# Kernel optimization log

Hardware: AMD Instinct MI355X
Metric: run time of the kernel (lower is better)

Reference implementation:

```python
import jax, jax.numpy as jnp
import numpy as np

# Config mirrors init_kwargs
D_IN, D_OUT, HEADS, SEQ, BATCH = 1024, 64, 16, 2048, 2


def setup_inputs() -> dict:
    key = jax.random.key(0)
    kx, kq, kk, kv = jax.random.split(key, 4)
    scale = 1.0 / np.sqrt(D_IN)
    x = jax.random.normal(kx, (BATCH, SEQ, D_IN), dtype=jnp.float32)
    # Stacked per-head projection weights, [H, d_in, d_out] (qkv_bias=False)
    Wq = jax.random.normal(kq, (HEADS, D_IN, D_OUT), dtype=jnp.float32) * scale
    Wk = jax.random.normal(kk, (HEADS, D_IN, D_OUT), dtype=jnp.float32) * scale
    Wv = jax.random.normal(kv, (HEADS, D_IN, D_OUT), dtype=jnp.float32) * scale
    return {"x": x, "Wq": Wq, "Wk": Wk, "Wv": Wv}


def reference(x, Wq, Wk, Wv):
    # x: [B, S, d_in]; W*: [H, d_in, d_out]
    q = jnp.einsum("bsd,hde->bhse", x, Wq)
    k = jnp.einsum("bsd,hde->bhse", x, Wk)
    v = jnp.einsum("bsd,hde->bhse", x, Wv)
    scores = jnp.einsum("bhse,bhte->bhst", q, k) / jnp.sqrt(
        jnp.asarray(D_OUT, dtype=q.dtype)
    )
    S = x.shape[1]
    causal = jnp.tril(jnp.ones((S, S), dtype=bool))  # [S, S]
    scores = jnp.where(causal[None, None], scores, -jnp.inf)
    attn = jax.nn.softmax(scores, axis=-1)  # dropout=0.0 (eval)
    ctx = jnp.einsum("bhst,bhte->bhse", attn, v)  # [B, H, S, d_out]
    # concat heads on last dim -> [B, S, H*d_out]
    B, H, S2, E = ctx.shape
    return jnp.transpose(ctx, (0, 2, 1, 3)).reshape(B, S2, H * E)
```

## Files before the change

### kernel.cpp

```cpp
#include <hip/hip_runtime.h>
#include <hip/hip_bf16.h>
#include <math.h>

#define BATCH 2
#define SEQ   2048
#define DIN   1024
#define HEADS 16
#define EDIM  64

#define NX   (BATCH*SEQ*DIN)
#define NW   (3*HEADS*DIN*EDIM)
#define NQKV (BATCH*HEADS*SEQ*EDIM)

#define QSCALE 0.18033688011112042f

typedef __attribute__((ext_vector_type(8))) short short8;
typedef __attribute__((ext_vector_type(4))) float f32x4;

static __device__ __forceinline__ ushort f2bf(float f) {
    __hip_bfloat16 h = __float2bfloat16(f);
    return *reinterpret_cast<ushort*>(&h);
}

static __device__ __forceinline__ void gload16(const void* g, void* l) {
    void* gv = const_cast<void*>(g);
    __builtin_amdgcn_global_load_lds(
        (__attribute__((address_space(1))) void*)gv,
        (__attribute__((address_space(3))) void*)l,
        16, 0, 0);
}

static __device__ __forceinline__ void barrier_fenced() {
    asm volatile("" ::: "memory");
    __builtin_amdgcn_s_barrier();
    asm volatile("" ::: "memory");
}

__global__ __launch_bounds__(256) void prep(
    const float* __restrict__ x, const float* __restrict__ Wq,
    const float* __restrict__ Wk, const float* __restrict__ Wv,
    ushort* __restrict__ xb, ushort* __restrict__ wt)
{
    const int t = threadIdx.x;
    if (blockIdx.x < 1024) {
        const int v0 = blockIdx.x * 256 + t;
#pragma unroll
        for (int i = 0; i < 4; ++i) {
            int i4 = (v0 + i * 262144) * 4;
            float4 f = *(const float4*)(x + i4);
            ushort4 o;
            o.x = f2bf(f.x); o.y = f2bf(f.y); o.z = f2bf(f.z); o.w = f2bf(f.w);
            *(ushort4*)(xb + i4) = o;
        }
    } else {
        const int bid = blockIdx.x - 1024;
        const int dt  = bid & 15;
        const int h   = (bid >> 4) & 15;
        const int mat = bid >> 8;

        const float* W = (mat == 0) ? Wq : (mat == 1) ? Wk : Wv;
        const float* src = W + ((size_t)h * DIN + dt * 64) * EDIM;
        ushort* dst = wt + ((size_t)(mat * HEADS + h) * EDIM) * DIN + dt * 64;

        __shared__ ushort T[64][68];
#pragma unroll
        for (int i = 0; i < 16; ++i) {
            int v = t + i * 256;
            int d = v >> 6, e = v & 63;
            T[d][e] = f2bf(src[(size_t)d * EDIM + e]);
        }
        __syncthreads();
#pragma unroll
        for (int i = 0; i < 4; ++i) {
            int v = t + i * 256;
            int e = v >> 4, d4 = (v & 15) << 2;
            ushort4 ov;
            ov.x = T[d4 + 0][e]; ov.y = T[d4 + 1][e];
            ov.z = T[d4 + 2][e]; ov.w = T[d4 + 3][e];
            *(ushort4*)&dst[(size_t)e * DIN + d4] = ov;
        }
    }
}

__global__ __launch_bounds__(256) void qkv_gemm(
    const ushort* __restrict__ xb, const ushort* __restrict__ wt,
    ushort* __restrict__ qkv)
{
    const int bid = blockIdx.x;
    const int xcd = bid & 7;
    const int idx = bid >> 3;
    const int mt  = (xcd >> 1) * 8 + idx / 12;
    const int nt  = (xcd & 1) * 12 + idx % 12;
    const int m0 = mt * 128, n0 = nt * 128;
    const int b  = mt >> 4;

    __shared__ ushort As[2][128][64];
    __shared__ ushort Bs[2][128][64];

    const int t    = threadIdx.x;
    const int lane = t & 63;
    const int w    = t >> 6;
    const int wr   = w >> 1, wc = w & 1;
    const int fr   = lane & 15;
    const int fk   = (lane >> 4) * 8;
    const int rg   = (lane >> 4) * 4;
    const int sw   = (fr & 7) << 3;

    const ushort* xbase = xb + (size_t)m0 * DIN;
    const ushort* wbase = wt + (size_t)n0 * DIN;

    const int lrow = lane >> 3;
    const int lcol = ((lane & 7) ^ (lane >> 3)) << 3;

#define STAGE(buf, k0)                                                          \
    {                                                                           \
        _Pragma("unroll")                                                       \
        for (int j = 0; j < 4; ++j) {                                           \
            const int c = w * 4 + j;                                            \
            gload16(&xbase[(size_t)(c * 8 + lrow) * DIN + (k0) + lcol], &As[buf][c * 8][0]); \
            gload16(&wbase[(size_t)(c * 8 + lrow) * DIN + (k0) + lcol], &Bs[buf][c * 8][0]); \
        }                                                                       \
    }

    f32x4 acc[4][4];
#pragma unroll
    for (int i = 0; i < 4; ++i)
#pragma unroll
        for (int j = 0; j < 4; ++j) acc[i][j] = (f32x4)0.f;

    STAGE(0, 0);
    STAGE(1, 64);

    short8 a[4][2], bfr[4][2];

#define LOAD_FRAGS(cur)                                                         \
    {                                                                           \
        _Pragma("unroll")                                                       \
        for (int rb = 0; rb < 4; ++rb)                                          \
            _Pragma("unroll")                                                   \
            for (int kk = 0; kk < 2; ++kk) {                                    \
                a[rb][kk]   = *(const short8*)&As[cur][wr * 64 + rb * 16 + fr][(kk * 32 + fk) ^ sw]; \
                bfr[rb][kk] = *(const short8*)&Bs[cur][wc * 64 + rb * 16 + fr][(kk * 32 + fk) ^ sw]; \
            }                                                                   \
    }

#define DO_MFMA()                                                               \
    {                                                                           \
        _Pragma("unroll")                                                       \
        for (int kk = 0; kk < 2; ++kk)                                          \
            _Pragma("unroll")                                                   \
            for (int rb = 0; rb < 4; ++rb)                                      \
                _Pragma("unroll")                                               \
                for (int cf = 0; cf < 4; ++cf)                                  \
                    acc[rb][cf] = __builtin_amdgcn_mfma_f32_16x16x32_bf16(a[rb][kk], bfr[cf][kk], acc[rb][cf], 0, 0, 0); \
    }

    for (int kt = 0; kt < 15; ++kt) {
        const int cur = kt & 1;

        asm volatile("s_waitcnt vmcnt(8)" ::: "memory");
        __builtin_amdgcn_sched_barrier(0);
        barrier_fenced();

        LOAD_FRAGS(cur);

        asm volatile("s_waitcnt lgkmcnt(0)" ::: "memory");
        __builtin_amdgcn_sched_barrier(0);
        barrier_fenced();

        if (kt <= 13) STAGE(cur, (kt + 2) * 64);

        DO_MFMA();
    }
    {
        asm volatile("s_waitcnt vmcnt(0)" ::: "memory");
        __builtin_amdgcn_sched_barrier(0);
        barrier_fenced();
        LOAD_FRAGS(1);
        DO_MFMA();
    }
#undef STAGE
#undef LOAD_FRAGS
#undef DO_MFMA

    const int hg  = nt * 2 + wc;
    const int mat = hg >> 4;
    const int h   = hg & 15;
    const int s0  = (m0 & 2047) + wr * 64;
    if (mat < 2) {
        const float sc = (mat == 0) ? QSCALE : 1.0f;
        ushort* dst = qkv + (size_t)mat * NQKV
                    + ((size_t)((b * HEADS + h) * SEQ) + s0) * EDIM;
#pragma unroll
        for (int rb = 0; rb < 4; ++rb)
#pragma unroll
            for (int cf = 0; cf < 4; ++cf)
#pragma unroll
                for (int i = 0; i < 4; ++i)
                    dst[(size_t)(rb * 16 + rg + i) * EDIM + cf * 16 + fr] = f2bf(acc[rb][cf][i] * sc);
    } else {
        ushort* vtb = qkv + (size_t)2 * NQKV + ((size_t)(b * HEADS + h) * EDIM) * SEQ;
#pragma unroll
        for (int rb = 0; rb < 4; ++rb)
#pragma unroll
            for (int cf = 0; cf < 4; ++cf) {
                ushort4 ov;
                ov.x = f2bf(acc[rb][cf][0]); ov.y = f2bf(acc[rb][cf][1]);
                ov.z = f2bf(acc[rb][cf][2]); ov.w = f2bf(acc[rb][cf][3]);
                *(ushort4*)&vtb[(size_t)(cf * 16 + fr) * SEQ + s0 + rb * 16 + rg] = ov;
            }
    }
}

__global__ __launch_bounds__(512) void flash_mfma(
    const ushort* __restrict__ q, const ushort* __restrict__ k,
    const ushort* __restrict__ vt, float* __restrict__ out)
{
    const int bid = blockIdx.x;
    const int bh  = bid & 31;
    const int b   = bh >> 4;
    const int h   = bh & 15;
    const int it  = (bid < 256) ? (15 - (bid >> 5)) : ((bid - 256) >> 5);
    const int KT  = 2 * it + 2;

    const ushort* Qb  = q  + ((size_t)((b * HEADS + h) * SEQ) + it * 128) * EDIM;
    const ushort* Kb  = k  + ((size_t)((b * HEADS + h) * SEQ)) * EDIM;
    const ushort* Vtb = vt + ((size_t)((b * HEADS + h) * EDIM)) * SEQ;

    __shared__ ushort Ks_[2][64][64];
    __shared__ ushort Vs_[2][64][64];
    __shared__ ushort Ps_[8][16][72];

    const int t    = threadIdx.x;
    const int lane = t & 63;
    const int w    = t >> 6;
    const int fr   = lane & 15;
    const int fk   = (lane >> 4) * 8;
    const int rg   = (lane >> 4) * 4;
    const int sw   = (fr & 7) << 3;

    const int srow8 = lane >> 3;
    const int sunit = (lane & 7) ^ srow8;

#define FSTAGE(buf, tile)                                                      \
    {                                                                          \
        gload16(&Kb[(size_t)((tile) * 64 + w * 8 + srow8) * EDIM + sunit * 8], \
                &Ks_[buf][w * 8][0]);                                          \
        gload16(&Vtb[(size_t)(w * 8 + srow8) * SEQ + (tile) * 64 + sunit * 8], \
                &Vs_[buf][w * 8][0]);                                          \
    }

    const int wrow0 = it * 128 + w * 16;
    const int lastT = wrow0 >> 6;
    const int qrow  = wrow0 + fr;

    short8 qf[2];
#pragma unroll
    for (int kk = 0; kk < 2; ++kk)
        qf[kk] = *(const short8*)&Qb[(size_t)(w * 16 + fr) * EDIM + kk * 32 + fk];
    asm volatile("s_waitcnt vmcnt(0)" ::: "memory");
    __builtin_amdgcn_sched_barrier(0);

    f32x4 o_[4];
#pragma unroll
    for (int cf = 0; cf < 4; ++cf) o_[cf] = (f32x4)0.f;
    float lpart = 0.f;

    FSTAGE(0, 0);

    for (int kt = 0; kt < KT; ++kt) {
        const int cur = kt & 1;

        asm volatile("s_waitcnt vmcnt(0)" ::: "memory");
        __builtin_amdgcn_sched_barrier(0);
        barrier_fenced();

        if (kt + 1 < KT) FSTAGE(cur ^ 1, kt + 1);

        if (kt <= lastT) {
            f32x4 s[4];
#pragma unroll
            for (int cf = 0; cf < 4; ++cf) s[cf] = (f32x4)0.f;
#pragma unroll
            for (int cf = 0; cf < 4; ++cf)
#pragma unroll
                for (int kk = 0; kk < 2; ++kk) {
                    short8 kf = *(const short8*)&Ks_[cur][cf * 16 + fr][(kk * 32 + fk) ^ sw];
                    s[cf] = __builtin_amdgcn_mfma_f32_16x16x32_bf16(kf, qf[kk], s[cf], 0, 0, 0);
                }

            if (kt == lastT) {
#pragma unroll
                for (int cf = 0; cf < 4; ++cf)
#pragma unroll
                    for (int i = 0; i < 4; ++i) {
                        int kpos = kt * 64 + cf * 16 + rg + i;
                        if (kpos > qrow) s[cf][i] = -1e30f;
                    }
            }

            float ls = 0.f;
#pragma unroll
            for (int cf = 0; cf < 4; ++cf) {
                float p0 = __builtin_amdgcn_exp2f(s[cf][0]);
                float p1 = __builtin_amdgcn_exp2f(s[cf][1]);
                float p2 = __builtin_amdgcn_exp2f(s[cf][2]);
                float p3 = __builtin_amdgcn_exp2f(s[cf][3]);
                ls += (p0 + p1) + (p2 + p3);
                uint2 pk;
                pk.x = (uint)f2bf(p0) | ((uint)f2bf(p1) << 16);
                pk.y = (uint)f2bf(p2) | ((uint)f2bf(p3) << 16);
                *(uint2*)&Ps_[w][fr][cf * 16 + rg] = pk;
            }
            lpart += ls;

            short8 pf[2];
#pragma unroll
            for (int kb = 0; kb < 2; ++kb)
                pf[kb] = *(const short8*)&Ps_[w][fr][kb * 32 + fk];
#pragma unroll
            for (int cf = 0; cf < 4; ++cf)
#pragma unroll
                for (int kb = 0; kb < 2; ++kb) {
                    short8 vf = *(const short8*)&Vs_[cur][cf * 16 + fr][(kb * 32 + fk) ^ sw];
                    o_[cf] = __builtin_amdgcn_mfma_f32_16x16x32_bf16(vf, pf[kb], o_[cf], 0, 0, 0);
                }
        }
    }
#undef FSTAGE

    float ls = lpart;
    ls += __shfl_xor(ls, 16);
    ls += __shfl_xor(ls, 32);
    const float inv = 1.f / ls;

    float* rowp = out + ((size_t)(b * SEQ + qrow)) * (HEADS * EDIM) + h * EDIM;
#pragma unroll
    for (int cf = 0; cf < 4; ++cf) {
        f32x4 ov = o_[cf] * inv;
        *(f32x4*)&rowp[cf * 16 + rg] = ov;
    }
}

extern "C" void kernel_launch(void* const* d_in, const int* in_sizes, int n_in,
                              void* d_out, int out_size, void* d_ws, size_t ws_size,
                              hipStream_t stream) {
    const float* x  = (const float*)d_in[0];
    const float* Wq = (const float*)d_in[1];
    const float* Wk = (const float*)d_in[2];
    const float* Wv = (const float*)d_in[3];
    float* out = (float*)d_out;

    ushort* xb  = (ushort*)d_ws;
    ushort* wt  = xb + NX;
    ushort* qkv = wt + NW;

    prep<<<1792, 256, 0, stream>>>(x, Wq, Wk, Wv, xb, wt);
    qkv_gemm<<<768, 256, 0, stream>>>(xb, wt, qkv);
    flash_mfma<<<BATCH * HEADS * (SEQ / 128), 512, 0, stream>>>(
        qkv, qkv + NQKV, qkv + (size_t)2 * NQKV, out);
}
```

Before: 85.55 us.

## Split long causal query tiles across two blocks and combine partial results

Query tiles 8-15, which have the longest key ranges, now have their key loop split across two work items, and a constant table balances per-block work to at most 16 key tiles. Split halves write unnormalized bf16 partial outputs and row sums to workspace, and a new combine kernel adds them and normalizes. The aim is to cut the tail caused by uneven causal work across 512 blocks. In exchange it adds a kernel launch, extra workspace traffic, and bf16 rounding of partial outputs before the combine. Merging without max rescaling is valid only because the softmax never subtracts a running max.

```diff
diff --git a/kernel.cpp b/kernel.cpp
--- a/kernel.cpp
+++ b/kernel.cpp
@@ -20,6 +20,10 @@
 static __device__ __forceinline__ ushort f2bf(float f) {
     __hip_bfloat16 h = __float2bfloat16(f);
     return *reinterpret_cast<ushort*>(&h);
+}
+static __device__ __forceinline__ float bf2f(ushort u) {
+    uint v = (uint)u << 16;
+    return *reinterpret_cast<float*>(&v);
 }
 
 static __device__ __forceinline__ void gload16(const void* g, void* l) {
@@ -35,6 +39,11 @@
     __builtin_amdgcn_s_barrier();
     asm volatile("" ::: "memory");
 }
+
+__constant__ int FT_IT[24]  = {15,15, 7,14,14,13,13, 6,12,12,11,11, 5,10,10, 9, 9, 4, 8, 8, 3, 2, 1, 0};
+__constant__ int FT_K0[24]  = { 0,16, 0, 0,15, 0,14, 0, 0,13, 0,12, 0, 0,11, 0,10, 0, 0, 9, 0, 0, 0, 0};
+__constant__ int FT_CNT[24] = {16,16,16,15,15,14,14,14,13,13,12,12,12,11,11,10,10,10, 9, 9, 8, 6, 4, 2};
+__constant__ int FT_SL[24]  = {14,15,-1,12,13,10,11,-1, 8, 9, 6, 7,-1, 4, 5, 2, 3,-1, 0, 1,-1,-1,-1,-1};
 
 __global__ __launch_bounds__(256) void prep(
     const float* __restrict__ x, const float* __restrict__ Wq,
@@ -212,16 +221,20 @@
     }
 }
 
-__global__ __launch_bounds__(512) void flash_mfma(
+__global__ __launch_bounds__(512) void flash_part(
     const ushort* __restrict__ q, const ushort* __restrict__ k,
-    const ushort* __restrict__ vt, float* __restrict__ out)
+    const ushort* __restrict__ vt, float* __restrict__ out,
+    ushort* __restrict__ pO, float* __restrict__ pl)
 {
-    const int bid = blockIdx.x;
-    const int bh  = bid & 31;
-    const int b   = bh >> 4;
-    const int h   = bh & 15;
-    const int it  = (bid < 256) ? (15 - (bid >> 5)) : ((bid - 256) >> 5);
-    const int KT  = 2 * it + 2;
+    const int bid  = blockIdx.x;
+    const int item = bid >> 5;
+    const int bh   = bid & 31;
+    const int b    = bh >> 4;
+    const int h    = bh & 15;
+    const int it   = FT_IT[item];
+    const int k0t  = FT_K0[item];
+    const int cnt  = FT_CNT[item];
+    const int slot = FT_SL[item];
 
     const ushort* Qb  = q  + ((size_t)((b * HEADS + h) * SEQ) + it * 128) * EDIM;
     const ushort* Kb  = k  + ((size_t)((b * HEADS + h) * SEQ)) * EDIM;
@@ -266,18 +279,19 @@
     for (int cf = 0; cf < 4; ++cf) o_[cf] = (f32x4)0.f;
     float lpart = 0.f;
 
-    FSTAGE(0, 0);
-
-    for (int kt = 0; kt < KT; ++kt) {
-        const int cur = kt & 1;
+    FSTAGE(0, k0t);
+
+    for (int ktl = 0; ktl < cnt; ++ktl) {
+        const int cur  = ktl & 1;
+        const int kt_g = k0t + ktl;
 
         asm volatile("s_waitcnt vmcnt(0)" ::: "memory");
         __builtin_amdgcn_sched_barrier(0);
         barrier_fenced();
 
-        if (kt + 1 < KT) FSTAGE(cur ^ 1, kt + 1);
-
-        if (kt <= lastT) {
+        if (ktl + 1 < cnt) FSTAGE(cur ^ 1, k0t + ktl + 1);
+
+        if (kt_g <= lastT) {
             f32x4 s[4];
 #pragma unroll
             for (int cf = 0; cf < 4; ++cf) s[cf] = (f32x4)0.f;
@@ -289,12 +303,12 @@
                     s[cf] = __builtin_amdgcn_mfma_f32_16x16x32_bf16(kf, qf[kk], s[cf], 0, 0, 0);
                 }
 
-            if (kt == lastT) {
+            if (kt_g == lastT) {
 #pragma unroll
                 for (int cf = 0; cf < 4; ++cf)
 #pragma unroll
                     for (int i = 0; i < 4; ++i) {
-                        int kpos = kt * 64 + cf * 16 + rg + i;
+                        int kpos = kt_g * 64 + cf * 16 + rg + i;
                         if (kpos > qrow) s[cf][i] = -1e30f;
                     }
             }
@@ -332,13 +346,54 @@
     float ls = lpart;
     ls += __shfl_xor(ls, 16);
     ls += __shfl_xor(ls, 32);
-    const float inv = 1.f / ls;
-
-    float* rowp = out + ((size_t)(b * SEQ + qrow)) * (HEADS * EDIM) + h * EDIM;
-#pragma unroll
-    for (int cf = 0; cf < 4; ++cf) {
-        f32x4 ov = o_[cf] * inv;
-        *(f32x4*)&rowp[cf * 16 + rg] = ov;
+
+    if (slot < 0) {
+        const float inv = 1.f / ls;
+        float* rowp = out + ((size_t)(b * SEQ + qrow)) * (HEADS * EDIM) + h * EDIM;
+#pragma unroll
+        for (int cf = 0; cf < 4; ++cf) {
+            f32x4 ov = o_[cf] * inv;
+            *(f32x4*)&rowp[cf * 16 + rg] = ov;
+        }
+    } else {
+        ushort* po = pO + (((size_t)bh * 16 + slot) * 128 + (w * 16 + fr)) * 64;
+#pragma unroll
+        for (int cf = 0; cf < 4; ++cf) {
+            ushort4 ov;
+            ov.x = f2bf(o_[cf][0]); ov.y = f2bf(o_[cf][1]);
+            ov.z = f2bf(o_[cf][2]); ov.w = f2bf(o_[cf][3]);
+            *(ushort4*)&po[cf * 16 + rg] = ov;
+        }
+        if ((lane >> 4) == 0)
+            pl[((size_t)bh * 16 + slot) * 128 + (w * 16 + fr)] = ls;
+    }
+}
+
+__global__ __launch_bounds__(256) void combine(
+    const ushort* __restrict__ pO, const float* __restrict__ pl,
+    float* __restrict__ out)
+{
+    const int bid = blockIdx.x;
+    const int bh  = bid & 31;
+    const int b   = bh >> 4;
+    const int h   = bh & 15;
+    const int it8 = bid >> 5;
+    const int it  = 8 + it8;
+
+    const ushort* p0 = pO + ((size_t)bh * 16 + it8 * 2) * (128 * 64);
+    const ushort* p1 = p0 + 128 * 64;
+    const float*  l0 = pl + ((size_t)bh * 16 + it8 * 2) * 128;
+    const float*  l1 = l0 + 128;
+
+    const int t  = threadIdx.x;
+    const int rr = t >> 6;
+    const int e  = t & 63;
+
+    for (int rb = 0; rb < 32; ++rb) {
+        int row = rb * 4 + rr;
+        float l = l0[row] + l1[row];
+        float o = bf2f(p0[row * 64 + e]) + bf2f(p1[row * 64 + e]);
+        out[((size_t)(b * SEQ + it * 128 + row)) * (HEADS * EDIM) + h * EDIM + e] = o / l;
     }
 }
 
@@ -354,9 +409,12 @@
     ushort* xb  = (ushort*)d_ws;
     ushort* wt  = xb + NX;
     ushort* qkv = wt + NW;
+    ushort* pO  = qkv + (size_t)3 * NQKV;
+    float*  pl  = (float*)(pO + (size_t)32 * 16 * 128 * 64);
 
     prep<<<1792, 256, 0, stream>>>(x, Wq, Wk, Wv, xb, wt);
     qkv_gemm<<<768, 256, 0, stream>>>(xb, wt, qkv);
-    flash_mfma<<<BATCH * HEADS * (SEQ / 128), 512, 0, stream>>>(
-        qkv, qkv + NQKV, qkv + (size_t)2 * NQKV, out);
-}
+    flash_part<<<768, 512, 0, stream>>>(
+        qkv, qkv + NQKV, qkv + (size_t)2 * NQKV, out, pO, pl);
+    combine<<<256, 256, 0, stream>>>(pO, pl, out);
+}
```

After: 81.43 us, median of 4. 1.05x faster.
